# Performance work log

Measured on AMD Instinct MI355X. Metric: run time of the kernel, lower is better.

## Reference

```python
import jax, jax.numpy as jnp
import numpy as np

N = 8192
F_IN = 690
F_OUT = 690
H = 3
ALPHA = 0.2  # LeakyReLU negative slope
NEG_INF = -9e15


def setup_inputs() -> dict:
    key = jax.random.key(0)
    k1, k2, k3, k4 = jax.random.split(key, 4)
    x = jax.random.normal(k1, (N, F_IN), dtype=jnp.float32)
    adj = jax.random.randint(k2, (N, N), 0, 2, dtype=jnp.int32)
    adj = adj.at[jnp.arange(N), jnp.arange(N)].set(1)  # self-loops, as in eye() init
    # Xavier-ish scaled params, stacked over heads
    W = jax.random.normal(k3, (H, F_IN, F_OUT), dtype=jnp.float32) * 0.05
    a = jax.random.normal(k4, (H, 2 * F_OUT, 1), dtype=jnp.float32) * 0.05
    return {"x": x, "adj": adj, "W": W, "a": a}


def reference(x, adj, W, a):
    # Wh per head: [H, N, F_OUT]
    Wh = jnp.einsum('nf,hfo->hno', x, W)
    # Additive decomposition of concat-based score: e_ij = leakyrelu(a1_i + a2_j)
    a1 = jnp.einsum('hno,ho->hn', Wh, a[:, :F_OUT, 0])  # [H, N]
    a2 = jnp.einsum('hno,ho->hn', Wh, a[:, F_OUT:, 0])  # [H, N]
    e = jax.nn.leaky_relu(a1[:, :, None] + a2[:, None, :], negative_slope=ALPHA)  # [H, N, N]
    e = jnp.where(adj[None, :, :] > 0, e, NEG_INF)
    attn = jax.nn.softmax(e, axis=-1)
    h_prime = jnp.einsum('hnm,hmo->hno', attn, Wh)  # [H, N, F_OUT]
    # GAT(concat=False): mean over heads, then ELU (dropout is identity in eval)
    y = jax.nn.elu(jnp.mean(h_prime, axis=0))  # [N, F_OUT]
    return y
```

## Files before the change

kernel.cpp:

```cpp
#include <hip/hip_runtime.h>
#include <hip/hip_bf16.h>
#include <stdint.h>

#define NN 8192
#define FD 690
#define NH 3
#define KPAD 704
#define OPAD 768
#define USTRIDE 704
#define KS 4
#define LOG2E 1.4426950408889634f

typedef __attribute__((ext_vector_type(8))) short bf16x8;
typedef __attribute__((ext_vector_type(4))) float f32x4;

typedef __attribute__((address_space(1))) const void gas_t;
typedef __attribute__((address_space(3))) void las_t;

__device__ __forceinline__ void async_ld16(const void* g, void* l) {
  __builtin_amdgcn_global_load_lds((gas_t*)g, (las_t*)l, 16, 0, 0);
}

__device__ __forceinline__ float bf2f(unsigned short u) {
  return __uint_as_float(((unsigned int)u) << 16);
}
__device__ __forceinline__ unsigned short f2bf(float f) {
  __hip_bfloat16 h = __float2bfloat16(f);
  return *reinterpret_cast<unsigned short*>(&h);
}
__device__ __forceinline__ float selbit(float e, uint32_t lo, uint32_t hi) {
  uint64_t m = ((uint64_t)hi << 32) | lo;
  float r;
  asm("v_cndmask_b32 %0, 0, %1, %2" : "=v"(r) : "v"(e), "s"(m));
  return r;
}

__global__ __launch_bounds__(256) void k_cast_x(const float* __restrict__ x,
                                                unsigned short* __restrict__ xb) {
  int idx = blockIdx.x * 256 + threadIdx.x;
  if (idx >= NN * KPAD) return;
  int n = idx / KPAD, f = idx - n * KPAD;
  float v = (f < FD) ? x[(size_t)n * FD + f] : 0.f;
  xb[idx] = f2bf(v);
}

__global__ __launch_bounds__(256) void k_cast_wt(const float* __restrict__ W,
                                                 unsigned short* __restrict__ wt) {
  int idx = blockIdx.x * 256 + threadIdx.x;
  if (idx >= NH * OPAD * KPAD) return;
  int h = idx / (OPAD * KPAD);
  int rem = idx - h * OPAD * KPAD;
  int o = rem / KPAD, f = rem - o * KPAD;
  float v = (o < FD && f < FD) ? W[((size_t)h * FD + f) * FD + o] : 0.f;
  wt[idx] = f2bf(v);
}

__global__ __launch_bounds__(256) void k_pack(const int* __restrict__ adj,
                                              uint64_t* __restrict__ bm) {
  int wid = (blockIdx.x * 256 + threadIdx.x) >> 6;
  int lane = threadIdx.x & 63;
  int i = wid >> 7, wj = wid & 127;
  int v = adj[(int64_t)i * NN + wj * 64 + lane];
  uint64_t m = __ballot(v > 0);
  if (lane == 0) bm[i * 128 + wj] = m;
}

__global__ __launch_bounds__(512) void k_gemm_wht(const unsigned short* __restrict__ wt,
                                                  const unsigned short* __restrict__ xb,
                                                  unsigned short* __restrict__ wht) {
  const int m0 = blockIdx.x * 128;
  const int n0 = blockIdx.y * 256;
  const int h  = blockIdx.z;
  const int tid = threadIdx.x;
  const int w = tid >> 6, l = tid & 63;
  const int wm = w >> 2, wn = w & 3;
  __shared__ unsigned short As[128 * 64];
  __shared__ unsigned short Bs[256 * 64];
  const unsigned short* Ag = wt + (size_t)h * OPAD * KPAD;
  f32x4 acc[4][4] = {};
  for (int kt = 0; kt < KPAD / 64; ++kt) {
    const int k0 = kt * 64;
#pragma unroll
    for (int r = 0; r < 2; ++r) {
      const unsigned short* g = Ag + (size_t)(m0 + r * 64 + w * 8 + (l >> 3)) * KPAD + k0 + (l & 7) * 8;
      async_ld16(g, &As[(r * 64 + w * 8) * 64]);
    }
#pragma unroll
    for (int r = 0; r < 4; ++r) {
      const unsigned short* g = xb + (size_t)(n0 + r * 64 + w * 8 + (l >> 3)) * KPAD + k0 + (l & 7) * 8;
      async_ld16(g, &Bs[(r * 64 + w * 8) * 64]);
    }
    __syncthreads();
#pragma unroll
    for (int ks = 0; ks < 2; ++ks) {
      bf16x8 af[4], bfr[4];
#pragma unroll
      for (int mi = 0; mi < 4; ++mi)
        af[mi] = *reinterpret_cast<const bf16x8*>(
            &As[(wm * 64 + mi * 16 + (l & 15)) * 64 + ks * 32 + (l >> 4) * 8]);
#pragma unroll
      for (int ni = 0; ni < 4; ++ni)
        bfr[ni] = *reinterpret_cast<const bf16x8*>(
            &Bs[(wn * 64 + ni * 16 + (l & 15)) * 64 + ks * 32 + (l >> 4) * 8]);
#pragma unroll
      for (int mi = 0; mi < 4; ++mi)
#pragma unroll
        for (int ni = 0; ni < 4; ++ni)
          acc[mi][ni] = __builtin_amdgcn_mfma_f32_16x16x32_bf16(af[mi], bfr[ni], acc[mi][ni], 0, 0, 0);
    }
    __syncthreads();
  }
  unsigned short* Wh = wht + (size_t)h * OPAD * NN;
#pragma unroll
  for (int mi = 0; mi < 4; ++mi)
#pragma unroll
    for (int j = 0; j < 4; ++j) {
      int o = m0 + wm * 64 + mi * 16 + (l >> 4) * 4 + j;
#pragma unroll
      for (int ni = 0; ni < 4; ++ni) {
        int n = n0 + wn * 64 + ni * 16 + (l & 15);
        float val = (o == FD) ? 1.0f : acc[mi][ni][j];
        Wh[(size_t)o * NN + n] = f2bf(val);
      }
    }
}

__global__ __launch_bounds__(256) void k_a1a2(const unsigned short* __restrict__ wht,
                                              const float* __restrict__ a,
                                              float* __restrict__ e1s, float* __restrict__ f1s,
                                              float* __restrict__ e2s, float* __restrict__ f2s) {
  const int h = blockIdx.y;
  const int n = blockIdx.x * 256 + threadIdx.x;
  const unsigned short* Wp = wht + (size_t)h * OPAD * NN + n;
  const float* ap = a + h * 2 * FD;
  float s1 = 0.f, s2 = 0.f;
  for (int o = 0; o < FD; ++o) {
    float wv = bf2f(Wp[(size_t)o * NN]);
    s1 += wv * ap[o];
    s2 += wv * ap[FD + o];
  }
  e1s[h * NN + n] = exp2f(s1 * LOG2E);
  f1s[h * NN + n] = exp2f(0.2f * s1 * LOG2E);
  e2s[h * NN + n] = exp2f(s2 * LOG2E);
  f2s[h * NN + n] = exp2f(0.2f * s2 * LOG2E);
}

__global__ __launch_bounds__(512) void k_pv(const unsigned short* __restrict__ wht,
                                            const float* __restrict__ e1s,
                                            const float* __restrict__ f1s,
                                            const float* __restrict__ e2s,
                                            const float* __restrict__ f2s,
                                            const uint64_t* __restrict__ bm,
                                            float* __restrict__ U) {
  const int m0 = blockIdx.x * 128;
  const int n0 = blockIdx.y * 256;
  const int h    = blockIdx.z / KS;
  const int kseg = blockIdx.z % KS;
  const int tid = threadIdx.x;
  const int w = tid >> 6, l = tid & 63;
  const int wu = __builtin_amdgcn_readfirstlane(w);
  const int wm = w >> 2, wn = w & 3;
  __shared__ unsigned short As[128 * 64];
  __shared__ unsigned short Bs[256 * 64];
  const unsigned short* Bg = wht + (size_t)h * OPAD * NN;
  const uint64_t* bmw = bm + (size_t)(m0 + wu * 16) * 128;
  float E1v[16], F1v[16];
#pragma unroll
  for (int r = 0; r < 16; ++r) {
    E1v[r] = e1s[h * NN + m0 + wu * 16 + r];
    F1v[r] = f1s[h * NN + m0 + wu * 16 + r];
  }
  f32x4 acc[4][4] = {};
  for (int kt = kseg * (NN / 64 / KS); kt < (kseg + 1) * (NN / 64 / KS); ++kt) {
    const int k0 = kt * 64;
#pragma unroll
    for (int r = 0; r < 4; ++r) {
      const unsigned short* g = Bg + (size_t)(n0 + r * 64 + wu * 8 + (l >> 3)) * NN
                                + k0 + ((l & 7) ^ (l >> 3)) * 8;
      async_ld16(g, &Bs[(r * 64 + wu * 8) * 64]);
    }
    const float e2v = e2s[h * NN + k0 + l];
    const float f2v = f2s[h * NN + k0 + l];
#pragma unroll
    for (int r = 0; r < 16; ++r) {
      uint64_t mrow = bmw[(size_t)r * 128 + kt];
      uint32_t mlo = __builtin_amdgcn_readfirstlane((uint32_t)mrow);
      uint32_t mhi = __builtin_amdgcn_readfirstlane((uint32_t)(mrow >> 32));
      float e = fmaxf(E1v[r] * e2v, F1v[r] * f2v);
      e = selbit(e, mlo, mhi);
      As[(wu * 16 + r) * 64 + (l ^ ((r & 7) << 3))] = f2bf(e);
    }
    __syncthreads();
#pragma unroll
    for (int ks = 0; ks < 2; ++ks) {
      bf16x8 af[4], bfr[4];
#pragma unroll
      for (int mi = 0; mi < 4; ++mi) {
        int row = wm * 64 + mi * 16 + (l & 15);
        af[mi] = *reinterpret_cast<const bf16x8*>(
            &As[row * 64 + (((ks * 4 + (l >> 4)) ^ (row & 7)) * 8)]);
      }
#pragma unroll
      for (int ni = 0; ni < 4; ++ni) {
        int row = wn * 64 + ni * 16 + (l & 15);
        bfr[ni] = *reinterpret_cast<const bf16x8*>(
            &Bs[row * 64 + (((ks * 4 + (l >> 4)) ^ (row & 7)) * 8)]);
      }
#pragma unroll
      for (int mi = 0; mi < 4; ++mi)
#pragma unroll
        for (int ni = 0; ni < 4; ++ni)
          acc[mi][ni] = __builtin_amdgcn_mfma_f32_16x16x32_bf16(af[mi], bfr[ni], acc[mi][ni], 0, 0, 0);
    }
    __syncthreads();
  }
#pragma unroll
  for (int mi = 0; mi < 4; ++mi)
#pragma unroll
    for (int j = 0; j < 4; ++j) {
      int i = m0 + wm * 64 + mi * 16 + (l >> 4) * 4 + j;
#pragma unroll
      for (int ni = 0; ni < 4; ++ni) {
        int n = n0 + wn * 64 + ni * 16 + (l & 15);
        if (n <= FD) unsafeAtomicAdd(&U[((size_t)h * NN + i) * USTRIDE + n], acc[mi][ni][j]);
      }
    }
}

__global__ __launch_bounds__(256) void k_final(const float* __restrict__ U,
                                               float* __restrict__ y) {
  int idx = blockIdx.x * 256 + threadIdx.x;
  if (idx >= NN * FD) return;
  int i = idx / FD, o = idx - i * FD;
  const size_t HS = (size_t)NN * USTRIDE;
  float s = 0.f;
#pragma unroll
  for (int h = 0; h < NH; ++h) {
    size_t b = h * HS + (size_t)i * USTRIDE;
    s += U[b + o] / U[b + FD];
  }
  s *= (1.f / 3.f);
  y[idx] = s > 0.f ? s : (expf(s) - 1.f);
}

extern "C" void kernel_launch(void* const* d_in, const int* in_sizes, int n_in,
                              void* d_out, int out_size, void* d_ws, size_t ws_size,
                              hipStream_t stream) {
  const float* x   = (const float*)d_in[0];
  const int*   adj = (const int*)d_in[1];
  const float* W   = (const float*)d_in[2];
  const float* a   = (const float*)d_in[3];
  float* y = (float*)d_out;

  char* ws = (char*)d_ws;
  size_t off = 0;
  auto alloc = [&](size_t bytes) {
    void* p = ws + off;
    off = (off + bytes + 255) & ~(size_t)255;
    return p;
  };
  unsigned short* xb  = (unsigned short*)alloc((size_t)NN * KPAD * 2);
  unsigned short* wt  = (unsigned short*)alloc((size_t)NH * OPAD * KPAD * 2);
  unsigned short* wht = (unsigned short*)alloc((size_t)NH * OPAD * NN * 2);
  float* e1s = (float*)alloc((size_t)NH * NN * 4);
  float* f1s = (float*)alloc((size_t)NH * NN * 4);
  float* e2s = (float*)alloc((size_t)NH * NN * 4);
  float* f2s = (float*)alloc((size_t)NH * NN * 4);
  uint64_t* bm = (uint64_t*)alloc((size_t)NN * 128 * 8);
  float* U = (float*)alloc((size_t)NH * NN * USTRIDE * 4);
  (void)ws_size; (void)in_sizes; (void)n_in; (void)out_size;

  k_cast_x<<<(NN * KPAD + 255) / 256, 256, 0, stream>>>(x, xb);
  k_cast_wt<<<(NH * OPAD * KPAD + 255) / 256, 256, 0, stream>>>(W, wt);
  k_pack<<<NN * 128 / 4, 256, 0, stream>>>(adj, bm);
  k_gemm_wht<<<dim3(OPAD / 128, NN / 256, NH), 512, 0, stream>>>(wt, xb, wht);
  k_a1a2<<<dim3(NN / 256, NH), 256, 0, stream>>>(wht, a, e1s, f1s, e2s, f2s);
  hipMemsetAsync(U, 0, (size_t)NH * NN * USTRIDE * 4, stream);
  k_pv<<<dim3(NN / 128, OPAD / 256, NH * KS), 512, 0, stream>>>(wht, e1s, f1s, e2s, f2s, bm, U);
  k_final<<<(NN * FD + 255) / 256, 256, 0, stream>>>(U, y);
}
```

Baseline: 649.2 us.

## Double-buffer B tiles in attention-PV kernel to overlap loads with compute

The B-operand shared-memory tile becomes two buffers. The async global-to-LDS load for the next k-tile is issued before the current tile's score computation and MFMA loop, and the full syncthreads are replaced by explicit waitcnt plus barrier. MFMA sections also raise wave priority. This is meant to hide global load latency behind compute. LDS use grows from 48KB to 80KB per block, which may reduce occupancy, and the correctness of the manual wait placement is a risk.

```diff
diff --git a/kernel.cpp b/kernel.cpp
--- a/kernel.cpp
+++ b/kernel.cpp
@@ -161,7 +161,7 @@
   const int wu = __builtin_amdgcn_readfirstlane(w);
   const int wm = w >> 2, wn = w & 3;
   __shared__ unsigned short As[128 * 64];
-  __shared__ unsigned short Bs[256 * 64];
+  __shared__ unsigned short Bs[2][256 * 64];
   const unsigned short* Bg = wht + (size_t)h * OPAD * NN;
   const uint64_t* bmw = bm + (size_t)(m0 + wu * 16) * 128;
   float E1v[16], F1v[16];
@@ -170,15 +170,32 @@
     E1v[r] = e1s[h * NN + m0 + wu * 16 + r];
     F1v[r] = f1s[h * NN + m0 + wu * 16 + r];
   }
-  f32x4 acc[4][4] = {};
-  for (int kt = kseg * (NN / 64 / KS); kt < (kseg + 1) * (NN / 64 / KS); ++kt) {
+
+  auto stage = [&](int buf, int kt) {
     const int k0 = kt * 64;
 #pragma unroll
     for (int r = 0; r < 4; ++r) {
       const unsigned short* g = Bg + (size_t)(n0 + r * 64 + wu * 8 + (l >> 3)) * NN
                                 + k0 + ((l & 7) ^ (l >> 3)) * 8;
-      async_ld16(g, &Bs[(r * 64 + wu * 8) * 64]);
-    }
+      async_ld16(g, &Bs[buf][(r * 64 + wu * 8) * 64]);
+    }
+  };
+
+  const int kt0 = kseg * (128 / KS);
+  const int ktend = kt0 + 128 / KS;
+
+  f32x4 acc[4][4] = {};
+
+  stage(0, kt0);
+  asm volatile("s_waitcnt vmcnt(0)" ::: "memory");
+  __builtin_amdgcn_s_barrier();
+  __builtin_amdgcn_sched_barrier(0);
+
+  int cur = 0;
+  for (int kt = kt0; kt < ktend; ++kt) {
+    if (kt + 1 < ktend) stage(cur ^ 1, kt + 1);
+
+    const int k0 = kt * 64;
     const float e2v = e2s[h * NN + k0 + l];
     const float f2v = f2s[h * NN + k0 + l];
 #pragma unroll
@@ -190,7 +207,12 @@
       e = selbit(e, mlo, mhi);
       As[(wu * 16 + r) * 64 + (l ^ ((r & 7) << 3))] = f2bf(e);
     }
-    __syncthreads();
+
+    asm volatile("s_waitcnt lgkmcnt(0)" ::: "memory");
+    __builtin_amdgcn_s_barrier();
+    __builtin_amdgcn_sched_barrier(0);
+
+    __builtin_amdgcn_s_setprio(1);
 #pragma unroll
     for (int ks = 0; ks < 2; ++ks) {
       bf16x8 af[4], bfr[4];
@@ -204,7 +226,7 @@
       for (int ni = 0; ni < 4; ++ni) {
         int row = wn * 64 + ni * 16 + (l & 15);
         bfr[ni] = *reinterpret_cast<const bf16x8*>(
-            &Bs[row * 64 + (((ks * 4 + (l >> 4)) ^ (row & 7)) * 8)]);
+            &Bs[cur][row * 64 + (((ks * 4 + (l >> 4)) ^ (row & 7)) * 8)]);
       }
 #pragma unroll
       for (int mi = 0; mi < 4; ++mi)
@@ -212,8 +234,14 @@
         for (int ni = 0; ni < 4; ++ni)
           acc[mi][ni] = __builtin_amdgcn_mfma_f32_16x16x32_bf16(af[mi], bfr[ni], acc[mi][ni], 0, 0, 0);
     }
-    __syncthreads();
-  }
+    __builtin_amdgcn_s_setprio(0);
+
+    asm volatile("s_waitcnt vmcnt(0) lgkmcnt(0)" ::: "memory");
+    __builtin_amdgcn_s_barrier();
+    __builtin_amdgcn_sched_barrier(0);
+    cur ^= 1;
+  }
+
 #pragma unroll
   for (int mi = 0; mi < 4; ++mi)
 #pragma unroll
```

Measured after the change: 827.8 us. 27.5% more time.

## Retile attention-value kernel to 64x384 tiles with fewer K splits

Applied to the files above, without the earlier changes.

Changes the k_pv tile from 128x256 to 64x384 (output width covered by two tiles instead of three), gives each wave a 64x48 strip, halves the K split count, and adds an occupancy hint to launch_bounds. The aim is to generate each attention tile once per two column tiles instead of three, and to cut atomic accumulation traffic into U. The trade-off is less reuse of the B operand, since tiles have fewer rows, and less parallelism across the K dimension.

```diff
diff --git a/kernel.cpp b/kernel.cpp
--- a/kernel.cpp
+++ b/kernel.cpp
@@ -8,7 +8,7 @@
 #define KPAD 704
 #define OPAD 768
 #define USTRIDE 704
-#define KS 4
+#define KS 2
 #define LOG2E 1.4426950408889634f
 
 typedef __attribute__((ext_vector_type(8))) short bf16x8;
@@ -145,83 +145,92 @@
   f2s[h * NN + n] = exp2f(0.2f * s2 * LOG2E);
 }
 
-__global__ __launch_bounds__(512) void k_pv(const unsigned short* __restrict__ wht,
-                                            const float* __restrict__ e1s,
-                                            const float* __restrict__ f1s,
-                                            const float* __restrict__ e2s,
-                                            const float* __restrict__ f2s,
-                                            const uint64_t* __restrict__ bm,
-                                            float* __restrict__ U) {
-  const int m0 = blockIdx.x * 128;
-  const int n0 = blockIdx.y * 256;
+__global__ __launch_bounds__(512, 4) void k_pv(const unsigned short* __restrict__ wht,
+                                               const float* __restrict__ e1s,
+                                               const float* __restrict__ f1s,
+                                               const float* __restrict__ e2s,
+                                               const float* __restrict__ f2s,
+                                               const uint64_t* __restrict__ bm,
+                                               float* __restrict__ U) {
+  const int m0 = blockIdx.x * 64;
+  const int n0 = blockIdx.y * 384;
   const int h    = blockIdx.z / KS;
   const int kseg = blockIdx.z % KS;
   const int tid = threadIdx.x;
   const int w = tid >> 6, l = tid & 63;
   const int wu = __builtin_amdgcn_readfirstlane(w);
-  const int wm = w >> 2, wn = w & 3;
-  __shared__ unsigned short As[128 * 64];
-  __shared__ unsigned short Bs[256 * 64];
+  __shared__ unsigned short As[64 * 64];
+  __shared__ unsigned short Bs[384 * 64];
   const unsigned short* Bg = wht + (size_t)h * OPAD * NN;
-  const uint64_t* bmw = bm + (size_t)(m0 + wu * 16) * 128;
-  float E1v[16], F1v[16];
-#pragma unroll
-  for (int r = 0; r < 16; ++r) {
-    E1v[r] = e1s[h * NN + m0 + wu * 16 + r];
-    F1v[r] = f1s[h * NN + m0 + wu * 16 + r];
-  }
-  f32x4 acc[4][4] = {};
-  for (int kt = kseg * (NN / 64 / KS); kt < (kseg + 1) * (NN / 64 / KS); ++kt) {
+  const uint64_t* bmw = bm + (size_t)(m0 + wu * 8) * 128;
+  float E1v[8], F1v[8];
+#pragma unroll
+  for (int r = 0; r < 8; ++r) {
+    E1v[r] = e1s[h * NN + m0 + wu * 8 + r];
+    F1v[r] = f1s[h * NN + m0 + wu * 8 + r];
+  }
+
+  const int kt0 = kseg * (NN / 64 / KS);
+  const int ktend = kt0 + NN / 64 / KS;
+
+  f32x4 acc[4][3] = {};
+
+  for (int kt = kt0; kt < ktend; ++kt) {
     const int k0 = kt * 64;
-#pragma unroll
-    for (int r = 0; r < 4; ++r) {
-      const unsigned short* g = Bg + (size_t)(n0 + r * 64 + wu * 8 + (l >> 3)) * NN
-                                + k0 + ((l & 7) ^ (l >> 3)) * 8;
-      async_ld16(g, &Bs[(r * 64 + wu * 8) * 64]);
-    }
     const float e2v = e2s[h * NN + k0 + l];
     const float f2v = f2s[h * NN + k0 + l];
 #pragma unroll
-    for (int r = 0; r < 16; ++r) {
+    for (int call = 0; call < 6; ++call) {
+      int c = call * 512 + tid;
+      int row = c >> 3;
+      int kb  = c & 7;
+      int kbs = kb ^ (row & 7);
+      const unsigned short* g = Bg + (size_t)(n0 + row) * NN + k0 + kbs * 8;
+      async_ld16(g, &Bs[(size_t)c * 8]);
+    }
+#pragma unroll
+    for (int r = 0; r < 8; ++r) {
       uint64_t mrow = bmw[(size_t)r * 128 + kt];
       uint32_t mlo = __builtin_amdgcn_readfirstlane((uint32_t)mrow);
       uint32_t mhi = __builtin_amdgcn_readfirstlane((uint32_t)(mrow >> 32));
       float e = fmaxf(E1v[r] * e2v, F1v[r] * f2v);
       e = selbit(e, mlo, mhi);
-      As[(wu * 16 + r) * 64 + (l ^ ((r & 7) << 3))] = f2bf(e);
-    }
-    __syncthreads();
+      As[(wu * 8 + r) * 64 + (l ^ (r << 3))] = f2bf(e);
+    }
+    __syncthreads();
+
 #pragma unroll
     for (int ks = 0; ks < 2; ++ks) {
-      bf16x8 af[4], bfr[4];
+      bf16x8 af[4], bfr[3];
 #pragma unroll
       for (int mi = 0; mi < 4; ++mi) {
-        int row = wm * 64 + mi * 16 + (l & 15);
+        int row = mi * 16 + (l & 15);
         af[mi] = *reinterpret_cast<const bf16x8*>(
             &As[row * 64 + (((ks * 4 + (l >> 4)) ^ (row & 7)) * 8)]);
       }
 #pragma unroll
-      for (int ni = 0; ni < 4; ++ni) {
-        int row = wn * 64 + ni * 16 + (l & 15);
+      for (int ni = 0; ni < 3; ++ni) {
+        int row = w * 48 + ni * 16 + (l & 15);
         bfr[ni] = *reinterpret_cast<const bf16x8*>(
             &Bs[row * 64 + (((ks * 4 + (l >> 4)) ^ (row & 7)) * 8)]);
       }
 #pragma unroll
       for (int mi = 0; mi < 4; ++mi)
 #pragma unroll
-        for (int ni = 0; ni < 4; ++ni)
+        for (int ni = 0; ni < 3; ++ni)
           acc[mi][ni] = __builtin_amdgcn_mfma_f32_16x16x32_bf16(af[mi], bfr[ni], acc[mi][ni], 0, 0, 0);
     }
     __syncthreads();
   }
+
 #pragma unroll
   for (int mi = 0; mi < 4; ++mi)
 #pragma unroll
     for (int j = 0; j < 4; ++j) {
-      int i = m0 + wm * 64 + mi * 16 + (l >> 4) * 4 + j;
-#pragma unroll
-      for (int ni = 0; ni < 4; ++ni) {
-        int n = n0 + wn * 64 + ni * 16 + (l & 15);
+      int i = m0 + mi * 16 + (l >> 4) * 4 + j;
+#pragma unroll
+      for (int ni = 0; ni < 3; ++ni) {
+        int n = n0 + w * 48 + ni * 16 + (l & 15);
         if (n <= FD) unsafeAtomicAdd(&U[((size_t)h * NN + i) * USTRIDE + n], acc[mi][ni][j]);
       }
     }
@@ -276,6 +285,6 @@
   k_gemm_wht<<<dim3(OPAD / 128, NN / 256, NH), 512, 0, stream>>>(wt, xb, wht);
   k_a1a2<<<dim3(NN / 256, NH), 256, 0, stream>>>(wht, a, e1s, f1s, e2s, f2s);
   hipMemsetAsync(U, 0, (size_t)NH * NN * USTRIDE * 4, stream);
-  k_pv<<<dim3(NN / 128, OPAD / 256, NH * KS), 512, 0, stream>>>(wht, e1s, f1s, e2s, f2s, bm, U);
+  k_pv<<<dim3(NN / 64, 2, NH * KS), 512, 0, stream>>>(wht, e1s, f1s, e2s, f2s, bm, U);
   k_final<<<(NN * FD + 255) / 256, 256, 0, stream>>>(U, y);
 }
```

After: 637.3 us. No clear change (-1.8%).
